# Optimization experiments

Hardware: AMD Instinct MI355X
Metric: run time of the kernel (lower is better)

Reference implementation:

```python
import jax, jax.numpy as jnp
import numpy as np


def setup_inputs() -> dict:
    key = jax.random.key(0)
    k1, k2, k3 = jax.random.split(key, 3)
    b, c, h, w = 4, 64, 64, 64
    content = jax.random.normal(k1, (b, c, h, w), dtype=jnp.float32)
    content_s = jax.random.normal(k2, (b, c, h, w), dtype=jnp.float32)
    style = jax.random.normal(k3, (b, c, h, w), dtype=jnp.float32)
    return {"content": content, "content_s": content_s, "style": style}


def reference(content, content_s, style):
    b, c, h, w = content.shape
    hw = h * w
    Fc = content.reshape(b, c, hw)      # [b, c, HW]
    Fs = content_s.reshape(b, c, hw)    # [b, c, HW]
    Fst = style.reshape(b, c, hw)       # [b, c, HW]
    # S[b, q, k] = sum_c Fc[b, c, q] * Fs[b, c, k]  (Fc transposed as in torch)
    S = jnp.einsum('bcq,bck->bqk', Fc, Fs)
    S = jax.nn.softmax(S, axis=-1)
    # O = style @ S^T : O[b, c, q] = sum_k Fst[b, c, k] * S[b, q, k]
    O = jnp.einsum('bck,bqk->bcq', Fst, S).reshape(b, c, h, w)
    return jnp.concatenate((content, O), axis=1)
```

## Files before the change

### kernel.cpp

```cpp
#include <hip/hip_runtime.h>
#include <math.h>


#define Bb 4
#define Cc 64
#define HWs 4096
#define SPLITS 8
#define TPS 8
#define RLOG2E 1.44269504088896340736f

typedef _Float16 half8 __attribute__((ext_vector_type(8)));
typedef _Float16 half4 __attribute__((ext_vector_type(4)));
typedef float floatx4 __attribute__((ext_vector_type(4)));

__global__ __launch_bounds__(256) void prep_k(const float* __restrict__ content,
                                              const float* __restrict__ Fs,
                                              const float* __restrict__ Fst,
                                              float* __restrict__ out,
                                              _Float16* __restrict__ Kt,
                                              _Float16* __restrict__ Vt) {
    const int bid = blockIdx.x;
    const int t = threadIdx.x;
    if (bid < 1024) {
        int i4 = bid * 256 + t;
        const float4* c4 = (const float4*)content;
        const float4* v4 = (const float4*)Fst;
        float4* o4 = (float4*)out;
        int b = i4 >> 16, rem = i4 & 65535;
        o4[(size_t)b * 131072 + rem] = c4[i4];
        float4 v = v4[i4];
        half4 h;
        h[0] = (_Float16)v.x; h[1] = (_Float16)v.y;
        h[2] = (_Float16)v.z; h[3] = (_Float16)v.w;
        *(half4*)(Vt + (size_t)i4 * 4) = h;
    } else {
        __shared__ _Float16 T[16][72];
        int e = bid - 1024;
        int b = e >> 8;
        int hw0 = (e & 255) * 16;
        const float* sb = Fs + (size_t)b * Cc * HWs;
        {
            int c = t >> 2, x4 = (t & 3) * 4;
            float4 v = *(const float4*)(sb + (size_t)c * HWs + hw0 + x4);
            T[x4 + 0][c] = (_Float16)v.x;
            T[x4 + 1][c] = (_Float16)v.y;
            T[x4 + 2][c] = (_Float16)v.z;
            T[x4 + 3][c] = (_Float16)v.w;
        }
        __syncthreads();
        if (t < 128) {
            int row = t >> 3, g = t & 7;
            _Float16* db = Kt + (size_t)b * HWs * Cc;
            *(half8*)(db + (size_t)(hw0 + row) * Cc + g * 8) = *(half8*)&T[row][g * 8];
        }
    }
}

__global__ __launch_bounds__(256, 2) void attn_k(const float* __restrict__ Fc,
                                                 const _Float16* __restrict__ Kt,
                                                 const _Float16* __restrict__ Vt,
                                                 _Float16* __restrict__ Opart,
                                                 float2* __restrict__ ml) {
    const int tid  = threadIdx.x;
    const int w    = tid >> 6;
    const int lane = tid & 63;
    const int quad = lane >> 4;
    const int l15  = lane & 15;
    const int qg = blockIdx.x & 15;
    const int b  = (blockIdx.x >> 4) & 3;
    const int s  = blockIdx.x >> 6;
    const int k0base = s * TPS * 64;
    const int qbase = qg * 256 + w * 64 + l15;

    __shared__ _Float16 Kl[2][64 * 64];
    __shared__ _Float16 Vl[2][64 * 64];
    __shared__ _Float16 Ps[4][2][16][72];

    const float*    Fcb = Fc + (size_t)b * Cc * HWs;
    const _Float16* Kb  = Kt + (size_t)b * HWs * Cc;
    const _Float16* Vb  = Vt + (size_t)b * Cc * HWs;

    const bool isK  = tid < 128;
    const int  sl   = tid & 127;
    const int  srow = sl >> 3;
    const int  sjg  = sl & 7;
    const int  ssw  = (sjg ^ (srow & 7)) * 8;

    half8 qf[4][2];
    #pragma unroll
    for (int g = 0; g < 4; ++g)
        #pragma unroll
        for (int j = 0; j < 8; ++j) {
            qf[g][0][j] = (_Float16)(Fcb[(size_t)(quad * 8 + j) * HWs + qbase + g * 16] * RLOG2E);
            qf[g][1][j] = (_Float16)(Fcb[(size_t)(32 + quad * 8 + j) * HWs + qbase + g * 16] * RLOG2E);
        }

    half8 st[4];
    auto stage_load = [&](int kt) {
        int kk0 = k0base + kt * 64;
        #pragma unroll
        for (int i = 0; i < 4; ++i) {
            int row = srow + 16 * i;
            if (isK) st[i] = *(const half8*)(Kb + (size_t)(kk0 + row) * 64 + sjg * 8);
            else     st[i] = *(const half8*)(Vb + (size_t)row * HWs + kk0 + sjg * 8);
        }
    };
    auto stage_write = [&](int p) {
        #pragma unroll
        for (int i = 0; i < 4; ++i) {
            int row = srow + 16 * i;
            if (isK) *(half8*)&Kl[p][row * 64 + ssw] = st[i];
            else     *(half8*)&Vl[p][row * 64 + ssw] = st[i];
        }
    };

    floatx4 acc[4][4];
    #pragma unroll
    for (int g = 0; g < 4; ++g)
        #pragma unroll
        for (int m = 0; m < 4; ++m) acc[g][m] = (floatx4)(0.0f);
    float m_run[4] = {-INFINITY, -INFINITY, -INFINITY, -INFINITY};
    float lsum[4] = {0.0f, 0.0f, 0.0f, 0.0f};

    stage_load(0);
    stage_write(0);
    stage_load(1);
    __syncthreads();

    const int swl = (l15 & 7);
    for (int kt = 0; kt < TPS; ++kt) {
        const int p = kt & 1;
        if (kt + 1 < TPS) stage_write(p ^ 1);
        if (kt + 2 < TPS) stage_load(kt + 2);

        half8 va[4][2];
        #pragma unroll
        for (int m = 0; m < 4; ++m)
            #pragma unroll
            for (int ks = 0; ks < 2; ++ks)
                va[m][ks] = *(const half8*)&Vl[p][(m * 16 + l15) * 64 + (((ks * 4 + quad) ^ swl) * 8)];

        #pragma unroll
        for (int h = 0; h < 2; ++h) {
            floatx4 sv[2][4];
            #pragma unroll
            for (int m = 0; m < 4; ++m) {
                half8 ka0 = *(const half8*)&Kl[p][(m * 16 + l15) * 64 + ((quad ^ swl) * 8)];
                half8 ka1 = *(const half8*)&Kl[p][(m * 16 + l15) * 64 + (((4 + quad) ^ swl) * 8)];
                #pragma unroll
                for (int u = 0; u < 2; ++u) {
                    const int g = h * 2 + u;
                    sv[u][m] = __builtin_amdgcn_mfma_f32_16x16x32_f16(ka0, qf[g][0], (floatx4)(0.0f), 0, 0, 0);
                    sv[u][m] = __builtin_amdgcn_mfma_f32_16x16x32_f16(ka1, qf[g][1], sv[u][m], 0, 0, 0);
                }
            }

            #pragma unroll
            for (int u = 0; u < 2; ++u) {
                const int g = h * 2 + u;
                float mx = -INFINITY;
                #pragma unroll
                for (int m = 0; m < 4; ++m)
                    #pragma unroll
                    for (int r = 0; r < 4; ++r) mx = fmaxf(mx, sv[u][m][r]);
                mx = fmaxf(mx, __shfl_xor(mx, 16));
                mx = fmaxf(mx, __shfl_xor(mx, 32));
                float m_new = fmaxf(m_run[g], mx);
                float alpha = exp2f(m_run[g] - m_new);
                m_run[g] = m_new;
                float part = 0.0f;
                #pragma unroll
                for (int m = 0; m < 4; ++m)
                    #pragma unroll
                    for (int r = 0; r < 4; ++r) {
                        float e = exp2f(sv[u][m][r] - m_new);
                        sv[u][m][r] = e;
                        part += e;
                    }
                lsum[g] = lsum[g] * alpha + part;
                #pragma unroll
                for (int m = 0; m < 4; ++m)
                    #pragma unroll
                    for (int r = 0; r < 4; ++r) acc[g][m][r] *= alpha;

                #pragma unroll
                for (int m = 0; m < 4; ++m) {
                    half4 pp;
                    pp[0] = (_Float16)sv[u][m][0]; pp[1] = (_Float16)sv[u][m][1];
                    pp[2] = (_Float16)sv[u][m][2]; pp[3] = (_Float16)sv[u][m][3];
                    *(half4*)&Ps[w][u][l15][m * 16 + quad * 4] = pp;
                }
                half8 pb0 = *(half8*)&Ps[w][u][l15][quad * 8];
                half8 pb1 = *(half8*)&Ps[w][u][l15][32 + quad * 8];

                #pragma unroll
                for (int m = 0; m < 4; ++m) {
                    acc[g][m] = __builtin_amdgcn_mfma_f32_16x16x32_f16(va[m][0], pb0, acc[g][m], 0, 0, 0);
                    acc[g][m] = __builtin_amdgcn_mfma_f32_16x16x32_f16(va[m][1], pb1, acc[g][m], 0, 0, 0);
                }
            }
        }

        __syncthreads();
    }

    _Float16* op = Opart + (((size_t)s * Bb + b) * Cc) * HWs;
    #pragma unroll
    for (int g = 0; g < 4; ++g) {
        lsum[g] += __shfl_xor(lsum[g], 16);
        lsum[g] += __shfl_xor(lsum[g], 32);
        int q = qbase + g * 16;
        #pragma unroll
        for (int m = 0; m < 4; ++m)
            #pragma unroll
            for (int r = 0; r < 4; ++r) {
                int c = m * 16 + quad * 4 + r;
                op[(size_t)c * HWs + q] = (_Float16)acc[g][m][r];
            }
        if (quad == 0)
            ml[((size_t)b * HWs + q) * SPLITS + s] = make_float2(m_run[g], lsum[g]);
    }
}

__global__ __launch_bounds__(256) void combine_k(const _Float16* __restrict__ Opart,
                                                 const float2* __restrict__ ml,
                                                 float* __restrict__ out) {
    int idx = blockIdx.x * 256 + threadIdx.x;
    int q = idx & 4095;
    int c = (idx >> 12) & 63;
    int b = idx >> 18;
    const float2* mlp = ml + ((size_t)b * HWs + q) * SPLITS;
    float2 mls[SPLITS];
    #pragma unroll
    for (int s = 0; s < SPLITS; ++s) mls[s] = mlp[s];
    float M = -INFINITY;
    #pragma unroll
    for (int s = 0; s < SPLITS; ++s) M = fmaxf(M, mls[s].x);
    float l = 0.0f, wgt[SPLITS];
    #pragma unroll
    for (int s = 0; s < SPLITS; ++s) {
        wgt[s] = exp2f(mls[s].x - M);
        l += wgt[s] * mls[s].y;
    }
    float o = 0.0f;
    #pragma unroll
    for (int s = 0; s < SPLITS; ++s)
        o += wgt[s] * (float)Opart[(((size_t)s * Bb + b) * Cc + c) * HWs + q];
    out[((size_t)b * 2 * Cc + Cc + c) * HWs + q] = o / l;
}

extern "C" void kernel_launch(void* const* d_in, const int* in_sizes, int n_in,
                              void* d_out, int out_size, void* d_ws, size_t ws_size,
                              hipStream_t stream) {
    const float* content   = (const float*)d_in[0];
    const float* content_s = (const float*)d_in[1];
    const float* style     = (const float*)d_in[2];
    float* out = (float*)d_out;

    _Float16* Kt = (_Float16*)d_ws;
    _Float16* Vt = Kt + (size_t)Bb * HWs * Cc;
    _Float16* Opart = Vt + (size_t)Bb * Cc * HWs;
    float2*   ml = (float2*)(Opart + (size_t)SPLITS * Bb * Cc * HWs);

    prep_k<<<dim3(2048), dim3(256), 0, stream>>>(content, content_s, style, out, Kt, Vt);
    attn_k<<<dim3(SPLITS * Bb * 16), dim3(256), 0, stream>>>(content, Kt, Vt, Opart, ml);
    combine_k<<<dim3(4096), dim3(256), 0, stream>>>(Opart, ml, out);
}
```

Baseline: 114.0 us.

## Split attention block across 8 waves with 32 queries each

Doubles the attention block to 512 threads (8 waves), with each wave handling 32 queries instead of 64. The block still covers 256 queries and shares the same K/V LDS tiles. Per-thread accumulators, Q fragments and staging registers are halved so the launch bound can ask for more resident waves, aiming for better latency hiding. The trade-off is that each K/V fragment read from LDS is now reused across only two query groups per wave instead of four, which raises LDS traffic per MFMA.

```diff
diff --git a/kernel.cpp b/kernel.cpp
--- a/kernel.cpp
+++ b/kernel.cpp
@@ -56,7 +56,7 @@
     }
 }
 
-__global__ __launch_bounds__(256, 2) void attn_k(const float* __restrict__ Fc,
+__global__ __launch_bounds__(512, 4) void attn_k(const float* __restrict__ Fc,
                                                  const _Float16* __restrict__ Kt,
                                                  const _Float16* __restrict__ Vt,
                                                  _Float16* __restrict__ Opart,
@@ -70,57 +70,57 @@
     const int b  = (blockIdx.x >> 4) & 3;
     const int s  = blockIdx.x >> 6;
     const int k0base = s * TPS * 64;
-    const int qbase = qg * 256 + w * 64 + l15;
+    const int qbase = qg * 256 + w * 32 + l15;
 
     __shared__ _Float16 Kl[2][64 * 64];
     __shared__ _Float16 Vl[2][64 * 64];
-    __shared__ _Float16 Ps[4][2][16][72];
+    __shared__ _Float16 Ps[8][16][72];
 
     const float*    Fcb = Fc + (size_t)b * Cc * HWs;
     const _Float16* Kb  = Kt + (size_t)b * HWs * Cc;
     const _Float16* Vb  = Vt + (size_t)b * Cc * HWs;
 
-    const bool isK  = tid < 128;
-    const int  sl   = tid & 127;
+    const bool isK  = tid < 256;
+    const int  sl   = tid & 255;
     const int  srow = sl >> 3;
     const int  sjg  = sl & 7;
     const int  ssw  = (sjg ^ (srow & 7)) * 8;
 
-    half8 qf[4][2];
-    #pragma unroll
-    for (int g = 0; g < 4; ++g)
+    half8 qf[2][2];
+    #pragma unroll
+    for (int g = 0; g < 2; ++g)
         #pragma unroll
         for (int j = 0; j < 8; ++j) {
             qf[g][0][j] = (_Float16)(Fcb[(size_t)(quad * 8 + j) * HWs + qbase + g * 16] * RLOG2E);
             qf[g][1][j] = (_Float16)(Fcb[(size_t)(32 + quad * 8 + j) * HWs + qbase + g * 16] * RLOG2E);
         }
 
-    half8 st[4];
+    half8 st[2];
     auto stage_load = [&](int kt) {
         int kk0 = k0base + kt * 64;
         #pragma unroll
-        for (int i = 0; i < 4; ++i) {
-            int row = srow + 16 * i;
+        for (int i = 0; i < 2; ++i) {
+            int row = srow + 32 * i;
             if (isK) st[i] = *(const half8*)(Kb + (size_t)(kk0 + row) * 64 + sjg * 8);
             else     st[i] = *(const half8*)(Vb + (size_t)row * HWs + kk0 + sjg * 8);
         }
     };
     auto stage_write = [&](int p) {
         #pragma unroll
-        for (int i = 0; i < 4; ++i) {
-            int row = srow + 16 * i;
+        for (int i = 0; i < 2; ++i) {
+            int row = srow + 32 * i;
             if (isK) *(half8*)&Kl[p][row * 64 + ssw] = st[i];
             else     *(half8*)&Vl[p][row * 64 + ssw] = st[i];
         }
     };
 
-    floatx4 acc[4][4];
-    #pragma unroll
-    for (int g = 0; g < 4; ++g)
+    floatx4 acc[2][4];
+    #pragma unroll
+    for (int g = 0; g < 2; ++g)
         #pragma unroll
         for (int m = 0; m < 4; ++m) acc[g][m] = (floatx4)(0.0f);
-    float m_run[4] = {-INFINITY, -INFINITY, -INFINITY, -INFINITY};
-    float lsum[4] = {0.0f, 0.0f, 0.0f, 0.0f};
+    float m_run[2] = {-INFINITY, -INFINITY};
+    float lsum[2] = {0.0f, 0.0f};
 
     stage_load(0);
     stage_write(0);
@@ -141,63 +141,55 @@
                 va[m][ks] = *(const half8*)&Vl[p][(m * 16 + l15) * 64 + (((ks * 4 + quad) ^ swl) * 8)];
 
         #pragma unroll
-        for (int h = 0; h < 2; ++h) {
-            floatx4 sv[2][4];
+        for (int g = 0; g < 2; ++g) {
+            floatx4 sv[4];
             #pragma unroll
             for (int m = 0; m < 4; ++m) {
                 half8 ka0 = *(const half8*)&Kl[p][(m * 16 + l15) * 64 + ((quad ^ swl) * 8)];
                 half8 ka1 = *(const half8*)&Kl[p][(m * 16 + l15) * 64 + (((4 + quad) ^ swl) * 8)];
+                sv[m] = __builtin_amdgcn_mfma_f32_16x16x32_f16(ka0, qf[g][0], (floatx4)(0.0f), 0, 0, 0);
+                sv[m] = __builtin_amdgcn_mfma_f32_16x16x32_f16(ka1, qf[g][1], sv[m], 0, 0, 0);
+            }
+
+            float mx = -INFINITY;
+            #pragma unroll
+            for (int m = 0; m < 4; ++m)
                 #pragma unroll
-                for (int u = 0; u < 2; ++u) {
-                    const int g = h * 2 + u;
-                    sv[u][m] = __builtin_amdgcn_mfma_f32_16x16x32_f16(ka0, qf[g][0], (floatx4)(0.0f), 0, 0, 0);
-                    sv[u][m] = __builtin_amdgcn_mfma_f32_16x16x32_f16(ka1, qf[g][1], sv[u][m], 0, 0, 0);
+                for (int r = 0; r < 4; ++r) mx = fmaxf(mx, sv[m][r]);
+            mx = fmaxf(mx, __shfl_xor(mx, 16));
+            mx = fmaxf(mx, __shfl_xor(mx, 32));
+            float m_new = fmaxf(m_run[g], mx);
+            float alpha = exp2f(m_run[g] - m_new);
+            m_run[g] = m_new;
+            float part = 0.0f;
+            #pragma unroll
+            for (int m = 0; m < 4; ++m)
+                #pragma unroll
+                for (int r = 0; r < 4; ++r) {
+                    float e = exp2f(sv[m][r] - m_new);
+                    sv[m][r] = e;
+                    part += e;
                 }
-            }
-
-            #pragma unroll
-            for (int u = 0; u < 2; ++u) {
-                const int g = h * 2 + u;
-                float mx = -INFINITY;
+            lsum[g] = lsum[g] * alpha + part;
+            #pragma unroll
+            for (int m = 0; m < 4; ++m)
                 #pragma unroll
-                for (int m = 0; m < 4; ++m)
-                    #pragma unroll
-                    for (int r = 0; r < 4; ++r) mx = fmaxf(mx, sv[u][m][r]);
-                mx = fmaxf(mx, __shfl_xor(mx, 16));
-                mx = fmaxf(mx, __shfl_xor(mx, 32));
-                float m_new = fmaxf(m_run[g], mx);
-                float alpha = exp2f(m_run[g] - m_new);
-                m_run[g] = m_new;
-                float part = 0.0f;
-                #pragma unroll
-                for (int m = 0; m < 4; ++m)
-                    #pragma unroll
-                    for (int r = 0; r < 4; ++r) {
-                        float e = exp2f(sv[u][m][r] - m_new);
-                        sv[u][m][r] = e;
-                        part += e;
-                    }
-                lsum[g] = lsum[g] * alpha + part;
-                #pragma unroll
-                for (int m = 0; m < 4; ++m)
-                    #pragma unroll
-                    for (int r = 0; r < 4; ++r) acc[g][m][r] *= alpha;
-
-                #pragma unroll
-                for (int m = 0; m < 4; ++m) {
-                    half4 pp;
-                    pp[0] = (_Float16)sv[u][m][0]; pp[1] = (_Float16)sv[u][m][1];
-                    pp[2] = (_Float16)sv[u][m][2]; pp[3] = (_Float16)sv[u][m][3];
-                    *(half4*)&Ps[w][u][l15][m * 16 + quad * 4] = pp;
-                }
-                half8 pb0 = *(half8*)&Ps[w][u][l15][quad * 8];
-                half8 pb1 = *(half8*)&Ps[w][u][l15][32 + quad * 8];
-
-                #pragma unroll
-                for (int m = 0; m < 4; ++m) {
-                    acc[g][m] = __builtin_amdgcn_mfma_f32_16x16x32_f16(va[m][0], pb0, acc[g][m], 0, 0, 0);
-                    acc[g][m] = __builtin_amdgcn_mfma_f32_16x16x32_f16(va[m][1], pb1, acc[g][m], 0, 0, 0);
-                }
+                for (int r = 0; r < 4; ++r) acc[g][m][r] *= alpha;
+
+            #pragma unroll
+            for (int m = 0; m < 4; ++m) {
+                half4 pp;
+                pp[0] = (_Float16)sv[m][0]; pp[1] = (_Float16)sv[m][1];
+                pp[2] = (_Float16)sv[m][2]; pp[3] = (_Float16)sv[m][3];
+                *(half4*)&Ps[w][l15][m * 16 + quad * 4] = pp;
+            }
+            half8 pb0 = *(half8*)&Ps[w][l15][quad * 8];
+            half8 pb1 = *(half8*)&Ps[w][l15][32 + quad * 8];
+
+            #pragma unroll
+            for (int m = 0; m < 4; ++m) {
+                acc[g][m] = __builtin_amdgcn_mfma_f32_16x16x32_f16(va[m][0], pb0, acc[g][m], 0, 0, 0);
+                acc[g][m] = __builtin_amdgcn_mfma_f32_16x16x32_f16(va[m][1], pb1, acc[g][m], 0, 0, 0);
             }
         }
 
@@ -206,7 +198,7 @@
 
     _Float16* op = Opart + (((size_t)s * Bb + b) * Cc) * HWs;
     #pragma unroll
-    for (int g = 0; g < 4; ++g) {
+    for (int g = 0; g < 2; ++g) {
         lsum[g] += __shfl_xor(lsum[g], 16);
         lsum[g] += __shfl_xor(lsum[g], 32);
         int q = qbase + g * 16;
@@ -263,6 +255,6 @@
     float2*   ml = (float2*)(Opart + (size_t)SPLITS * Bb * Cc * HWs);
 
     prep_k<<<dim3(2048), dim3(256), 0, stream>>>(content, content_s, style, out, Kt, Vt);
-    attn_k<<<dim3(SPLITS * Bb * 16), dim3(256), 0, stream>>>(content, Kt, Vt, Opart, ml);
+    attn_k<<<dim3(SPLITS * Bb * 16), dim3(512), 0, stream>>>(content, Kt, Vt, Opart, ml);
     combine_k<<<dim3(4096), dim3(256), 0, stream>>>(Opart, ml, out);
 }
```

Measured after the change: 133.6 us. +17.2%, slower.
